# Kernel optimization log

Measured on AMD Instinct MI355X. Metric: run time of the kernel, lower is better.

The kernel has to match this reference:

```python
import jax, jax.numpy as jnp
import numpy as np
from jax import lax

B, N, HID, H, FFN, L, MHD = 16, 128, 768, 32, 3072, 12, 5
S = N + 1


def _ln(x, g, b):
    m = x.mean(-1, keepdims=True)
    v = ((x - m) ** 2).mean(-1, keepdims=True)
    return (x - m) * lax.rsqrt(v + 1e-5) * g + b


def setup_inputs() -> dict:
    key = jax.random.key(0)
    ks = jax.random.split(key, 32)
    f = lambda i, shape: jax.random.normal(ks[i], shape, jnp.float32) * 0.02
    z0 = lambda w: w.at[0].set(0.0)  # padding_idx=0 rows are zero
    inp = {}
    inp["attn_bias"] = jax.random.normal(ks[0], (B, S, S), jnp.float32)
    inp["spatial_pos"] = jax.random.randint(ks[1], (B, N, N), 0, 512)
    inp["x"] = jax.random.randint(ks[2], (B, N, 9), 0, 4608)
    inp["in_degree"] = jax.random.randint(ks[3], (B, N), 0, 512)
    inp["out_degree"] = jax.random.randint(ks[4], (B, N), 0, 512)
    inp["edge_input"] = jax.random.randint(ks[5], (B, N, N, MHD, 3), 0, 1536)
    inp["atom_emb"] = z0(f(6, (512 * 9 + 1, HID)))
    inp["edge_emb"] = z0(f(7, (512 * 3 + 1, H)))
    inp["edge_dis_emb"] = f(8, (128 * H * H, 1))
    inp["spatial_emb"] = z0(f(9, (512, H)))
    inp["in_deg_emb"] = z0(f(10, (512, HID)))
    inp["out_deg_emb"] = z0(f(11, (512, HID)))
    inp["graph_token"] = f(12, (1, HID))
    inp["gt_vd"] = f(13, (1, H))
    inp["ln1_g"] = jnp.ones((L, HID)); inp["ln1_b"] = jnp.zeros((L, HID))
    inp["wq"] = f(14, (L, HID, HID)); inp["bq"] = jnp.zeros((L, HID))
    inp["wk"] = f(15, (L, HID, HID)); inp["bk"] = jnp.zeros((L, HID))
    inp["wv"] = f(16, (L, HID, HID)); inp["bv"] = jnp.zeros((L, HID))
    inp["wo"] = f(17, (L, HID, HID)); inp["bo"] = jnp.zeros((L, HID))
    inp["ln2_g"] = jnp.ones((L, HID)); inp["ln2_b"] = jnp.zeros((L, HID))
    inp["w1"] = f(18, (L, HID, FFN)); inp["b1"] = jnp.zeros((L, FFN))
    inp["w2"] = f(19, (L, FFN, HID)); inp["b2"] = jnp.zeros((L, HID))
    inp["final_g"] = jnp.ones((HID,)); inp["final_b"] = jnp.zeros((HID,))
    inp["proj_w"] = f(20, (HID, 1)); inp["proj_b"] = jnp.zeros((1,))
    return inp


def _forward(attn_bias, spatial_pos, x, in_degree, out_degree, edge_input,
             atom_emb, edge_emb, edge_dis_emb, spatial_emb, in_deg_emb, out_deg_emb,
             graph_token, gt_vd, ln1_g, ln1_b, wq, bq, wk, bk, wv, bv, wo, bo,
             ln2_g, ln2_b, w1, b1, w2, b2, final_g, final_b, proj_w, proj_b):
    Bn = attn_bias.shape[0]
    # ---- graph attention bias [B,H,S,S] ----
    gab = jnp.broadcast_to(attn_bias[:, None], (Bn, H, S, S))
    sp_bias = spatial_emb[spatial_pos].transpose(0, 3, 1, 2)  # [B,H,N,N]
    gab = gab.at[:, :, 1:, 1:].add(sp_bias)
    t = gt_vd.reshape(1, H, 1)
    gab = gab.at[:, :, 1:, 0].add(t)
    gab = gab.at[:, :, 0, :].add(t)
    # ---- multi-hop edge bias ----
    sp = jnp.where(spatial_pos == 0, 1, spatial_pos)
    sp = jnp.where(sp > 1, sp - 1, sp)
    sp = jnp.clip(sp, 0, MHD)
    ei = edge_input[:, :, :, :MHD, :]                  # [B,N,N,D,3]
    ee = edge_emb[ei].mean(-2)                         # [B,N,N,D,H]
    D = ee.shape[3]
    flat = ee.transpose(3, 0, 1, 2, 4).reshape(D, -1, H)
    W = edge_dis_emb.reshape(-1, H, H)[:D]
    flat = jnp.einsum('dbh,dhk->dbk', flat, W)
    ee = flat.reshape(D, Bn, N, N, H).transpose(1, 2, 3, 0, 4)
    ee = ee.sum(-2) / sp.astype(ee.dtype)[..., None]   # [B,N,N,H]
    gab = gab.at[:, :, 1:, 1:].add(ee.transpose(0, 3, 1, 2))
    gab = gab + attn_bias[:, None]
    # ---- node features ----
    nf = atom_emb[x].sum(-2) + in_deg_emb[in_degree] + out_deg_emb[out_degree]
    gt = jnp.broadcast_to(graph_token[None], (Bn, 1, HID))
    h = jnp.concatenate([gt, nf], axis=1)              # [B,S,HID]
    d = HID // H
    scale = d ** -0.5

    def step(h, p):
        g1, b1_, Wq, Bq, Wk, Bk, Wv, Bv, Wo, Bo, g2, b2_, W1, B1, W2, B2 = p
        y = _ln(h, g1, b1_)
        q = (y @ Wq + Bq).reshape(Bn, S, H, d) * scale
        k = (y @ Wk + Bk).reshape(Bn, S, H, d)
        v = (y @ Wv + Bv).reshape(Bn, S, H, d)
        s = jnp.einsum('bqhd,bkhd->bhqk', q, k) + gab
        a = jax.nn.softmax(s, axis=-1)
        o = jnp.einsum('bhqk,bkhd->bqhd', a, v).reshape(Bn, S, HID) @ Wo + Bo
        h = h + o
        z = _ln(h, g2, b2_)
        z = jax.nn.gelu(z @ W1 + B1, approximate=False) @ W2 + B2
        return h + z, None

    h = lax.scan(step, h, (ln1_g, ln1_b, wq, bq, wk, bk, wv, bv, wo, bo,
                           ln2_g, ln2_b, w1, b1, w2, b2))[0]
    h = _ln(h, final_g, final_b)
    return h[:, 0, :] @ proj_w + proj_b                # [B, output_dim]


def reference(attn_bias, spatial_pos, x, in_degree, out_degree, edge_input,
              atom_emb, edge_emb, edge_dis_emb, spatial_emb, in_deg_emb, out_deg_emb,
              graph_token, gt_vd, ln1_g, ln1_b, wq, bq, wk, bk, wv, bv, wo, bo,
              ln2_g, ln2_b, w1, b1, w2, b2, final_g, final_b, proj_w, proj_b):
    return _forward(attn_bias, spatial_pos, x, in_degree, out_degree, edge_input,
                    atom_emb, edge_emb, edge_dis_emb, spatial_emb, in_deg_emb, out_deg_emb,
                    graph_token, gt_vd, ln1_g, ln1_b, wq, bq, wk, bk, wv, bv, wo, bo,
                    ln2_g, ln2_b, w1, b1, w2, b2, final_g, final_b, proj_w, proj_b)
```

## Files before the change

### kernel.cpp

```cpp
#include <hip/hip_runtime.h>
#include <hip/hip_bf16.h>
#include <math.h>

#define B_ 16
#define N_ 128
#define S_ 129
#define HID_ 768
#define H_ 32
#define D_ 24
#define FFN_ 3072
#define L_ 12
#define M_ (B_*S_)
#define SP_ 144
#define KP_ 160

#define WQKV_E ((size_t)2304*768)
#define WO_E   ((size_t)768*768)
#define W1_E   ((size_t)3072*768)
#define W2_E   ((size_t)768*3072)
#define WL_E_  (WQKV_E + WO_E + W1_E + W2_E)

typedef __attribute__((ext_vector_type(8))) short short8;
typedef __attribute__((ext_vector_type(4))) float f32x4;
typedef __hip_bfloat16 bf16;

#define VMCNT(n) asm volatile("s_waitcnt vmcnt(" #n ")" ::: "memory")
#define LDS_FENCE() asm volatile("" ::: "memory")

__device__ __forceinline__ void gload_lds16(const void* g, void* l) {
  __builtin_amdgcn_global_load_lds(
      (const __attribute__((address_space(1))) void*)g,
      (__attribute__((address_space(3))) void*)l, 16, 0, 0);
}

__device__ __forceinline__ float gld(const float* p) { return *p; }
__device__ __forceinline__ float gld(const bf16* p)  { return __bfloat162float(*p); }

__global__ __launch_bounds__(256) void gab_bound_kernel(
    const float* __restrict__ ab, const float* __restrict__ gtvd,
    float* __restrict__ gab, bf16* __restrict__ gabh)
{
  int u = blockIdx.x * 256 + threadIdx.x;
  const int PB = 2*S_ - 1;
  if (u >= B_*H_*PB) return;
  int p = u % PB;
  int bh = u / PB;
  int hh = bh % H_, b = bh / H_;
  int qi, kj;
  if (p < S_) { qi = 0; kj = p; } else { qi = p - S_ + 1; kj = 0; }
  float v = 2.0f * ab[(b*S_ + qi)*S_ + kj] + gtvd[hh];
  long g = ((long)(b*H_ + hh)*S_ + qi)*S_ + kj;
  if (gabh) gabh[g] = __float2bfloat16(v);
  else      gab[g]  = v;
}

__global__ __launch_bounds__(256) void ftab_kernel(
    const float* __restrict__ eemb, const float* __restrict__ edis,
    float* __restrict__ F)
{
  __shared__ float em[8][32];
  int tid = threadIdx.x;
  int jl = tid >> 5, hh = tid & 31;
  int p = blockIdx.x * 8 + jl;
  bool valid = p < 5*1537;
  int d = valid ? p / 1537 : 0;
  int idx = valid ? p % 1537 : 0;
  em[jl][hh] = eemb[idx*32 + hh];
  float acc = 0.f;
#pragma unroll
  for (int hp = 0; hp < 32; ++hp)
    acc += em[jl][hp] * edis[d*1024 + hp*32 + hh];
  if (valid) F[(long)p*32 + hh] = acc * (1.0f/3.0f);
}

__global__ __launch_bounds__(256) void edge_kernel(
    const int* __restrict__ eidx, const float* __restrict__ F,
    const int* __restrict__ spos, const float* __restrict__ spemb,
    const float* __restrict__ ab, float* __restrict__ gab,
    bf16* __restrict__ gabh)
{
  __shared__ float outj[128][33];
  int tid = threadIdx.x;
  int jl = tid >> 5, hh = tid & 31;
  int bi = blockIdx.x;
  int b = bi >> 7, i = bi & 127;
  const int* erow = eidx + ((long)((b*N_ + i)*N_)) * 15;

  int er[15];
#pragma unroll
  for (int t = 0; t < 15; ++t) er[t] = erow[jl*15 + t];

  for (int ch = 0; ch < 16; ++ch) {
    int j = ch*8 + jl;
    int ern[15];
    if (ch < 15) {
#pragma unroll
      for (int t = 0; t < 15; ++t) ern[t] = erow[(j+8)*15 + t];
    }
    float acc = 0.f;
#pragma unroll
    for (int t = 0; t < 15; ++t)
      acc += F[((long)((t/3)*1537 + er[t]))*32 + hh];
    int sp0 = spos[(b*N_ + i)*N_ + j];
    int sp = (sp0 == 0) ? 1 : sp0;
    if (sp > 1) sp -= 1;
    if (sp > 5) sp = 5;
    outj[j][hh] = spemb[sp0*H_ + hh] + acc / (float)sp;
    if (ch < 15) {
#pragma unroll
      for (int t = 0; t < 15; ++t) er[t] = ern[t];
    }
  }
  __syncthreads();
  {
    int c = tid & 127;
    float base = 2.0f * ab[((long)(b*S_) + (i+1))*S_ + 1 + c];
    for (int it = 0; it < 16; ++it) {
      int r = it*2 + (tid >> 7);
      float v = base + outj[c][r];
      long g = ((long)(b*H_ + r)*S_ + (i+1))*S_ + 1 + c;
      if (gabh) gabh[g] = __float2bfloat16(v);
      else      gab[g]  = v;
    }
  }
}

__global__ __launch_bounds__(256) void nodefeat_ln_kernel(
    const int* __restrict__ x, const int* __restrict__ indeg,
    const int* __restrict__ outdeg, const float* __restrict__ atom_emb,
    const float* __restrict__ in_emb, const float* __restrict__ out_emb,
    const float* __restrict__ gtok, const float* __restrict__ g,
    const float* __restrict__ bta, float* __restrict__ h,
    bf16* __restrict__ y)
{
  int row = blockIdx.x;
  int tid = threadIdx.x;
  int sidx = row % S_;
  int b = row / S_;
  float v[3];
  if (sidx == 0) {
#pragma unroll
    for (int j = 0; j < 3; ++j) v[j] = gtok[tid + j*256];
  } else {
    int n = sidx - 1;
    int id = indeg[b*N_ + n], od = outdeg[b*N_ + n];
    const int* xr = x + (b*N_ + n)*9;
    int xi[9];
#pragma unroll
    for (int e = 0; e < 9; ++e) xi[e] = xr[e];
#pragma unroll
    for (int j = 0; j < 3; ++j) {
      int c = tid + j*256;
      float a = in_emb[(long)id*HID_ + c] + out_emb[(long)od*HID_ + c];
#pragma unroll
      for (int e = 0; e < 9; ++e) a += atom_emb[(long)xi[e]*HID_ + c];
      v[j] = a;
    }
  }
  float* hr = h + (long)row*HID_;
#pragma unroll
  for (int j = 0; j < 3; ++j) hr[tid + j*256] = v[j];

  float s = v[0] + v[1] + v[2];
  float ss = v[0]*v[0] + v[1]*v[1] + v[2]*v[2];
  for (int off = 32; off > 0; off >>= 1) {
    s  += __shfl_xor(s, off);
    ss += __shfl_xor(ss, off);
  }
  __shared__ float rs[4], rss[4];
  int w = tid / 64;
  if ((tid & 63) == 0) { rs[w] = s; rss[w] = ss; }
  __syncthreads();
  s  = rs[0] + rs[1] + rs[2] + rs[3];
  ss = rss[0] + rss[1] + rss[2] + rss[3];
  float mean = s * (1.0f/768.0f);
  float var  = ss * (1.0f/768.0f) - mean*mean;
  float rstd = rsqrtf(var + 1e-5f);
  bf16* yr = y + (long)row*HID_;
#pragma unroll
  for (int j = 0; j < 3; ++j) {
    int c = tid + j*256;
    yr[c] = __float2bfloat16((v[j] - mean)*rstd*g[c] + bta[c]);
  }
}

__global__ __launch_bounds__(256) void ln_kernel(
    const float* __restrict__ in, const float* __restrict__ g,
    const float* __restrict__ bta, bf16* __restrict__ out)
{
  int row = blockIdx.x;
  int tid = threadIdx.x;
  const float* xr = in + (long)row * HID_;
  float x0 = xr[tid], x1 = xr[tid + 256], x2 = xr[tid + 512];
  float s = x0 + x1 + x2;
  float ss = x0*x0 + x1*x1 + x2*x2;
  for (int off = 32; off > 0; off >>= 1) {
    s  += __shfl_xor(s, off);
    ss += __shfl_xor(ss, off);
  }
  __shared__ float rs[4], rss[4];
  int w = tid / 64;
  if ((tid & 63) == 0) { rs[w] = s; rss[w] = ss; }
  __syncthreads();
  s  = rs[0] + rs[1] + rs[2] + rs[3];
  ss = rss[0] + rss[1] + rss[2] + rss[3];
  float mean = s * (1.0f/768.0f);
  float var  = ss * (1.0f/768.0f) - mean*mean;
  float rstd = rsqrtf(var + 1e-5f);
  bf16* orow = out + (long)row * HID_;
  orow[tid]       = __float2bfloat16((x0 - mean)*rstd*g[tid]       + bta[tid]);
  orow[tid + 256] = __float2bfloat16((x1 - mean)*rstd*g[tid + 256] + bta[tid + 256]);
  orow[tid + 512] = __float2bfloat16((x2 - mean)*rstd*g[tid + 512] + bta[tid + 512]);
}

template<int NZ>
__global__ __launch_bounds__(256) void addln_kernel(
    const float* __restrict__ part, const float* __restrict__ bias,
    const float* __restrict__ g, const float* __restrict__ bta,
    float* __restrict__ h, bf16* __restrict__ y)
{
  int row = blockIdx.x;
  int tid = threadIdx.x;
  const long MN = (long)M_*HID_;
  float* hr = h + (long)row*HID_;
  float v[3];
#pragma unroll
  for (int j = 0; j < 3; ++j) {
    int c = tid + j*256;
    float a = hr[c] + bias[c];
    const float* pp = part + (long)row*HID_ + c;
#pragma unroll
    for (int z = 0; z < NZ; ++z) a += pp[(long)z*MN];
    v[j] = a;
    hr[c] = a;
  }
  float s = v[0] + v[1] + v[2];
  float ss = v[0]*v[0] + v[1]*v[1] + v[2]*v[2];
  for (int off = 32; off > 0; off >>= 1) {
    s  += __shfl_xor(s, off);
    ss += __shfl_xor(ss, off);
  }
  __shared__ float rs[4], rss[4];
  int w = tid / 64;
  if ((tid & 63) == 0) { rs[w] = s; rss[w] = ss; }
  __syncthreads();
  s  = rs[0] + rs[1] + rs[2] + rs[3];
  ss = rss[0] + rss[1] + rss[2] + rss[3];
  float mean = s * (1.0f/768.0f);
  float var  = ss * (1.0f/768.0f) - mean*mean;
  float rstd = rsqrtf(var + 1e-5f);
  bf16* yr = y + (long)row*HID_;
#pragma unroll
  for (int j = 0; j < 3; ++j) {
    int c = tid + j*256;
    yr[c] = __float2bfloat16((v[j] - mean)*rstd*g[c] + bta[c]);
  }
}

__global__ __launch_bounds__(256) void wconv_kernel(
    const float* __restrict__ W, bf16* __restrict__ Out,
    int K, int N, float scale)
{
  __shared__ float tile[32][33];
  int bx = blockIdx.x * 32;
  int by = blockIdx.y * 32;
  int tx = threadIdx.x & 31, ty = threadIdx.x >> 5;
#pragma unroll
  for (int r = 0; r < 32; r += 8)
    tile[ty + r][tx] = W[(long)(by + ty + r)*N + bx + tx];
  __syncthreads();
#pragma unroll
  for (int r = 0; r < 32; r += 8)
    Out[(long)(bx + ty + r)*K + by + tx] = __float2bfloat16(tile[tx][ty + r] * scale);
}

__global__ __launch_bounds__(256) void qkvconv_kernel(
    const float* __restrict__ wq, const float* __restrict__ wk,
    const float* __restrict__ wv, bf16* __restrict__ Out, float scale)
{
  const float* W = blockIdx.z == 0 ? wq : blockIdx.z == 1 ? wk : wv;
  float sc = blockIdx.z == 0 ? scale : 1.0f;
  __shared__ float tile[32][33];
  int bx = blockIdx.x * 32;
  int by = blockIdx.y * 32;
  int tx = threadIdx.x & 31, ty = threadIdx.x >> 5;
#pragma unroll
  for (int r = 0; r < 32; r += 8)
    tile[ty + r][tx] = W[(long)(by + ty + r)*768 + bx + tx];
  __syncthreads();
  bf16* O = Out + (long)blockIdx.z * 768 * 768;
#pragma unroll
  for (int r = 0; r < 32; r += 8)
    O[(long)(bx + ty + r)*768 + by + tx] = __float2bfloat16(tile[tx][ty + r] * sc);
}

__global__ __launch_bounds__(256) void qkvconv_all_kernel(
    const float* __restrict__ wq, const float* __restrict__ wk,
    const float* __restrict__ wv, bf16* __restrict__ wbuf, float scale)
{
  int z = blockIdx.z;
  int l = z / 3, which = z % 3;
  const float* W = (which == 0 ? wq : which == 1 ? wk : wv) + (size_t)l*768*768;
  float sc = which == 0 ? scale : 1.0f;
  __shared__ float tile[32][33];
  int bx = blockIdx.x * 32;
  int by = blockIdx.y * 32;
  int tx = threadIdx.x & 31, ty = threadIdx.x >> 5;
#pragma unroll
  for (int r = 0; r < 32; r += 8)
    tile[ty + r][tx] = W[(long)(by + ty + r)*768 + bx + tx];
  __syncthreads();
  bf16* O = wbuf + (size_t)l*WL_E_ + (size_t)which*768*768;
#pragma unroll
  for (int r = 0; r < 32; r += 8)
    O[(long)(bx + ty + r)*768 + by + tx] = __float2bfloat16(tile[tx][ty + r] * sc);
}

__global__ __launch_bounds__(256) void wconv_all_kernel(
    const float* __restrict__ Wb, bf16* __restrict__ Ob,
    int K, int N, long inStride, long outStride)
{
  int z = blockIdx.z;
  const float* W = Wb + (size_t)z * inStride;
  bf16* Out = Ob + (size_t)z * outStride;
  __shared__ float tile[32][33];
  int bx = blockIdx.x * 32;
  int by = blockIdx.y * 32;
  int tx = threadIdx.x & 31, ty = threadIdx.x >> 5;
#pragma unroll
  for (int r = 0; r < 32; r += 8)
    tile[ty + r][tx] = W[(long)(by + ty + r)*N + bx + tx];
  __syncthreads();
#pragma unroll
  for (int r = 0; r < 32; r += 8)
    Out[(long)(bx + ty + r)*K + by + tx] = __float2bfloat16(tile[tx][ty + r]);
}

__global__ __launch_bounds__(256) void biasqkv_kernel(
    const float* __restrict__ bq, const float* __restrict__ bk,
    const float* __restrict__ bv, float* __restrict__ bqkv, float scale)
{
  int idx = blockIdx.x * 256 + threadIdx.x;
  if (idx >= L_*2304) return;
  int l = idx / 2304, n = idx % 2304;
  int p = n / 768, nn = n % 768;
  float v = (p == 0) ? bq[l*768 + nn]*scale : (p == 1) ? bk[l*768 + nn] : bv[l*768 + nn];
  bqkv[idx] = v;
}

__device__ __forceinline__ void stage64k(
    const bf16* __restrict__ A, const bf16* __restrict__ Wt,
    bf16* Als, bf16* Bls, int bm, int bn, long ka, int M, int lda, int ldb, int tid)
{
  int r0 = tid >> 3, c = tid & 7;
#pragma unroll
  for (int p = 0; p < 2; ++p) {
    int row = p*32 + r0;
    int cs = c ^ (row & 7);
    int grow = bm + row; if (grow >= M) grow = M - 1;
    gload_lds16(A + (long)grow*lda + ka + cs*8, Als + (p*256 + (tid & ~63))*8);
    gload_lds16(Wt + (long)(bn + row)*ldb + ka + cs*8, Bls + (p*256 + (tid & ~63))*8);
  }
}

__global__ __launch_bounds__(256) void gemm64_kernel(
    const bf16* __restrict__ A, const bf16* __restrict__ Wt,
    const float* __restrict__ bias, const float* __restrict__ resid,
    void* __restrict__ Cout, int M, int N, int Klen, int lda, int ldb, int mode)
{
  constexpr int ASZ = 64*64;
  __shared__ bf16 Als[2*ASZ];
  __shared__ bf16 Bls[2*ASZ];
  int tid = threadIdx.x;
  int wid = tid >> 6, lane = tid & 63;

  int gx = gridDim.x;
  int nwg = gx * gridDim.y;
  int id = blockIdx.y * gx + blockIdx.x;
  int q = nwg >> 3, r = nwg & 7;
  int xcd = id & 7, off = id >> 3;
  int swz = (xcd < r) ? (xcd*(q+1) + off) : (r*(q+1) + (xcd - r)*q + off);
  int bm = (swz / gx) * 64, bn = (swz % gx) * 64;

  long koff = (long)blockIdx.z * Klen;
  int wr = wid >> 1, wc = wid & 1;
  int lr = lane & 15, kg = lane >> 4;

  int aoff[2][2], boff[2][2];
#pragma unroll
  for (int m = 0; m < 2; ++m) {
    int row = wr*32 + m*16 + lr;
#pragma unroll
    for (int hf = 0; hf < 2; ++hf) {
      int chunk = hf*4 + kg;
      aoff[m][hf] = (row*8 + (chunk ^ (row & 7)))*8;
    }
  }
#pragma unroll
  for (int n = 0; n < 2; ++n) {
    int col = wc*32 + n*16 + lr;
#pragma unroll
    for (int hf = 0; hf < 2; ++hf) {
      int chunk = hf*4 + kg;
      boff[n][hf] = (col*8 + (chunk ^ (col & 7)))*8;
    }
  }

  f32x4 acc[2][2];
#pragma unroll
  for (int m = 0; m < 2; ++m)
#pragma unroll
    for (int n = 0; n < 2; ++n)
      acc[m][n] = (f32x4){0.0f, 0.0f, 0.0f, 0.0f};

  int nt = Klen >> 6;
  stage64k(A, Wt, Als,       Bls,       bm, bn, koff,      M, lda, ldb, tid);
  stage64k(A, Wt, Als + ASZ, Bls + ASZ, bm, bn, koff + 64, M, lda, ldb, tid);

  int cur = 0;
  for (int t = 0; t < nt; ++t) {
    if (t + 1 < nt) VMCNT(4);
    else            VMCNT(0);
    __builtin_amdgcn_s_barrier();
    LDS_FENCE();
    bf16* Acur = Als + cur*ASZ;
    bf16* Bcur = Bls + cur*ASZ;
    short8 av[2][2], bv2[2][2];
#pragma unroll
    for (int m = 0; m < 2; ++m)
#pragma unroll
      for (int hf = 0; hf < 2; ++hf) av[m][hf] = *(const short8*)(Acur + aoff[m][hf]);
#pragma unroll
    for (int n = 0; n < 2; ++n)
#pragma unroll
      for (int hf = 0; hf < 2; ++hf) bv2[n][hf] = *(const short8*)(Bcur + boff[n][hf]);
#pragma unroll
    for (int hf = 0; hf < 2; ++hf)
#pragma unroll
      for (int m = 0; m < 2; ++m)
#pragma unroll
        for (int n = 0; n < 2; ++n)
          acc[m][n] = __builtin_amdgcn_mfma_f32_16x16x32_bf16(av[m][hf], bv2[n][hf], acc[m][n], 0, 0, 0);
    LDS_FENCE();
    __builtin_amdgcn_s_barrier();
    if (t + 2 < nt)
      stage64k(A, Wt, Als + cur*ASZ, Bls + cur*ASZ,
               bm, bn, koff + (long)(t+2)*64, M, lda, ldb, tid);
    cur ^= 1;
  }

#pragma unroll
  for (int n = 0; n < 2; ++n) {
    int col = bn + wc*32 + n*16 + lr;
    float bcol = (mode == 3) ? 0.0f : bias[col];
#pragma unroll
    for (int m = 0; m < 2; ++m) {
      f32x4 a = acc[m][n];
#pragma unroll
      for (int i = 0; i < 4; ++i) {
        int row = bm + wr*32 + m*16 + kg*4 + i;
        if (row < M) {
          float v = a[i] + bcol;
          if (mode == 1) v = 0.5f * v * (1.0f + erff(v * 0.70710678118654752f));
          if (mode == 2)
            ((float*)Cout)[(long)row*N + col] = v + resid[(long)row*N + col];
          else if (mode == 3)
            ((float*)Cout + (size_t)blockIdx.z*M*N)[(long)row*N + col] = v;
          else
            ((bf16*)Cout)[(long)row*N + col] = __float2bfloat16(v);
        }
      }
    }
  }
}

template<typename GT>
__global__ __launch_bounds__(512) void attn_kernel(
    const bf16* __restrict__ qkv, const GT* __restrict__ gab,
    bf16* __restrict__ ob)
{
  int bh = blockIdx.x;
  int b = bh >> 5, hh = bh & 31;
  __shared__ bf16 kl[SP_*32];
  __shared__ bf16 vt[32*KP_];
  __shared__ bf16 pl[8][16*KP_];
  int tid = threadIdx.x;
  int wv = tid >> 6, lane = tid & 63;
  const short8 z8 = (short8){0,0,0,0,0,0,0,0};

  for (int idx = tid; idx < 32*KP_/8; idx += 512)
    *(short8*)&vt[idx*8] = z8;
  const bf16* qbase = qkv + (long)b*S_*2304 + hh*24;
  for (int u = tid; u < SP_*4; u += 512) {
    int row = u >> 2, c8 = u & 3;
    short8 kv = z8;
    if (row < S_ && c8 < 3)
      kv = *(const short8*)(qbase + (long)row*2304 + 768 + c8*8);
    int cs = c8 ^ ((row >> 1) & 3);
    *(short8*)&kl[row*32 + cs*8] = kv;
  }
  __syncthreads();
  for (int u = tid; u < S_*3; u += 512) {
    int kj = u / 3, c8 = u % 3;
    short8 vv = *(const short8*)(qbase + (long)kj*2304 + 1536 + c8*8);
    int kb = kj & 7, kh = kj >> 3;
#pragma unroll
    for (int e = 0; e < 8; ++e) {
      int c = c8*8 + e;
      int ch = kh ^ ((c >> 1) & 3);
      short sv = vv[e];
      vt[c*KP_ + ch*8 + kb] = *reinterpret_cast<bf16*>(&sv);
    }
  }
  __syncthreads();

  int l15 = lane & 15, l4 = lane >> 4;

  short8 bvf[5][2];
#pragma unroll
  for (int kc = 0; kc < 5; ++kc)
#pragma unroll
    for (int ntc = 0; ntc < 2; ++ntc) {
      int col = ntc*16 + l15;
      int ch = (kc*4 + l4) ^ ((col >> 1) & 3);
      bvf[kc][ntc] = *(const short8*)&vt[col*KP_ + ch*8];
    }

  bf16* plw = pl[wv];
  for (int idx = lane; idx < 16*KP_/8; idx += 64)
    *(short8*)&plw[idx*8] = z8;

  const GT* gb = gab + (long)(b*H_ + hh)*S_*S_;

  for (int rep = 0; rep < 2; ++rep) {
    int mf = (rep == 0) ? wv : ((wv == 0) ? 8 : -1);
    if (mf < 0) continue;
    int qb0 = mf * 16;
    int qrow = qb0 + l15;
    short8 aq = z8;
    if (qrow < S_ && l4 < 3)
      aq = *(const short8*)(qbase + (long)qrow*2304 + l4*8);
    f32x4 sc[9];
#pragma unroll
    for (int nt = 0; nt < 9; ++nt) {
      int krow = nt*16 + l15;
      int kch = l4 ^ ((krow >> 1) & 3);
      short8 bk = *(const short8*)&kl[krow*32 + kch*8];
      sc[nt] = __builtin_amdgcn_mfma_f32_16x16x32_bf16(aq, bk, (f32x4){0,0,0,0}, 0, 0, 0);
    }
    float mx[4] = {-1e30f,-1e30f,-1e30f,-1e30f};
#pragma unroll
    for (int nt = 0; nt < 9; ++nt) {
      int kj = nt*16 + l15;
      int kjc = kj < S_ ? kj : 0;
#pragma unroll
      for (int i = 0; i < 4; ++i) {
        int q = qb0 + l4*4 + i;
        int qc = q < S_ ? q : 0;
        float v = sc[nt][i] + gld(&gb[(long)qc*S_ + kjc]);
        if (kj >= S_) v = -1e30f;
        sc[nt][i] = v;
        mx[i] = fmaxf(mx[i], v);
      }
    }
#pragma unroll
    for (int i = 0; i < 4; ++i) {
      mx[i] = fmaxf(mx[i], __shfl_xor(mx[i], 1));
      mx[i] = fmaxf(mx[i], __shfl_xor(mx[i], 2));
      mx[i] = fmaxf(mx[i], __shfl_xor(mx[i], 4));
      mx[i] = fmaxf(mx[i], __shfl_xor(mx[i], 8));
    }
    float sum[4] = {0.f,0.f,0.f,0.f};
#pragma unroll
    for (int nt = 0; nt < 9; ++nt)
#pragma unroll
      for (int i = 0; i < 4; ++i) {
        float e = __expf(sc[nt][i] - mx[i]);
        sc[nt][i] = e;
        sum[i] += e;
      }
#pragma unroll
    for (int i = 0; i < 4; ++i) {
      sum[i] += __shfl_xor(sum[i], 1);
      sum[i] += __shfl_xor(sum[i], 2);
      sum[i] += __shfl_xor(sum[i], 4);
      sum[i] += __shfl_xor(sum[i], 8);
    }
#pragma unroll
    for (int nt = 0; nt < 9; ++nt) {
      int kj = nt*16 + l15;
#pragma unroll
      for (int i = 0; i < 4; ++i) {
        int q = l4*4 + i;
        int ch = (kj >> 3) ^ ((q >> 1) & 3);
        plw[q*KP_ + ch*8 + (kj & 7)] = __float2bfloat16(sc[nt][i]);
      }
    }
    f32x4 av[2] = {(f32x4){0,0,0,0}, (f32x4){0,0,0,0}};
#pragma unroll
    for (int kc = 0; kc < 5; ++kc) {
      int ch = (kc*4 + l4) ^ ((l15 >> 1) & 3);
      short8 ap = *(const short8*)&plw[l15*KP_ + ch*8];
#pragma unroll
      for (int ntc = 0; ntc < 2; ++ntc)
        av[ntc] = __builtin_amdgcn_mfma_f32_16x16x32_bf16(ap, bvf[kc][ntc], av[ntc], 0, 0, 0);
    }
#pragma unroll
    for (int ntc = 0; ntc < 2; ++ntc) {
      int c = ntc*16 + l15;
      if (c < 24) {
#pragma unroll
        for (int i = 0; i < 4; ++i) {
          int q = qb0 + l4*4 + i;
          if (q < S_)
            ob[(long)(b*S_ + q)*768 + hh*24 + c] = __float2bfloat16(av[ntc][i] / sum[i]);
        }
      }
    }
  }
}

__global__ __launch_bounds__(256) void final_kernel(
    const float* __restrict__ h, const float* __restrict__ fg,
    const float* __restrict__ fb, const float* __restrict__ pw,
    const float* __restrict__ pb, float* __restrict__ out)
{
  int b = blockIdx.x;
  int tid = threadIdx.x;
  const float* xr = h + (long)b * S_ * HID_;
  float x0 = xr[tid], x1 = xr[tid + 256], x2 = xr[tid + 512];
  float s = x0 + x1 + x2;
  float ss = x0*x0 + x1*x1 + x2*x2;
  for (int off = 32; off > 0; off >>= 1) {
    s  += __shfl_xor(s, off);
    ss += __shfl_xor(ss, off);
  }
  __shared__ float rs[4], rss[4], rd[4];
  int w = tid / 64;
  if ((tid & 63) == 0) { rs[w] = s; rss[w] = ss; }
  __syncthreads();
  s  = rs[0] + rs[1] + rs[2] + rs[3];
  ss = rss[0] + rss[1] + rss[2] + rss[3];
  float mean = s * (1.0f/768.0f);
  float var  = ss * (1.0f/768.0f) - mean*mean;
  float rstd = rsqrtf(var + 1e-5f);
  float d0 = ((x0 - mean)*rstd*fg[tid]       + fb[tid])       * pw[tid];
  float d1 = ((x1 - mean)*rstd*fg[tid + 256] + fb[tid + 256]) * pw[tid + 256];
  float d2 = ((x2 - mean)*rstd*fg[tid + 512] + fb[tid + 512]) * pw[tid + 512];
  float pd = d0 + d1 + d2;
  for (int off = 32; off > 0; off >>= 1) pd += __shfl_xor(pd, off);
  if ((tid & 63) == 0) rd[w] = pd;
  __syncthreads();
  if (tid == 0) out[b] = rd[0] + rd[1] + rd[2] + rd[3] + pb[0];
}

extern "C" void kernel_launch(void* const* d_in, const int* in_sizes, int n_in,
                              void* d_out, int out_size, void* d_ws, size_t ws_size,
                              hipStream_t stream)
{
  const float* attn_bias   = (const float*)d_in[0];
  const int*   spatial_pos = (const int*)d_in[1];
  const int*   x           = (const int*)d_in[2];
  const int*   in_degree   = (const int*)d_in[3];
  const int*   out_degree  = (const int*)d_in[4];
  const int*   edge_input  = (const int*)d_in[5];
  const float* atom_emb    = (const float*)d_in[6];
  const float* edge_emb    = (const float*)d_in[7];
  const float* edge_dis    = (const float*)d_in[8];
  const float* spatial_emb = (const float*)d_in[9];
  const float* in_deg_emb  = (const float*)d_in[10];
  const float* out_deg_emb = (const float*)d_in[11];
  const float* graph_token = (const float*)d_in[12];
  const float* gt_vd       = (const float*)d_in[13];
  const float* ln1_g = (const float*)d_in[14];
  const float* ln1_b = (const float*)d_in[15];
  const float* wq = (const float*)d_in[16];
  const float* bq = (const float*)d_in[17];
  const float* wk = (const float*)d_in[18];
  const float* bk = (const float*)d_in[19];
  const float* wv = (const float*)d_in[20];
  const float* bv = (const float*)d_in[21];
  const float* wo = (const float*)d_in[22];
  const float* bo = (const float*)d_in[23];
  const float* ln2_g = (const float*)d_in[24];
  const float* ln2_b = (const float*)d_in[25];
  const float* w1 = (const float*)d_in[26];
  const float* b1 = (const float*)d_in[27];
  const float* w2 = (const float*)d_in[28];
  const float* b2 = (const float*)d_in[29];
  const float* final_g = (const float*)d_in[30];
  const float* final_b = (const float*)d_in[31];
  const float* proj_w  = (const float*)d_in[32];
  const float* proj_b  = (const float*)d_in[33];

  float* out = (float*)d_out;

  const float scale = 0.20412414523193154f;
  const long GAB_N = (long)B_*H_*S_*S_;
  const size_t PART_B = (size_t)4 * M_ * 768 * 4;

  char* dws = (char*)d_ws;
  char* p = dws;
  float* gab  = (float*)p;  p += GAB_N*4;
  float* h    = (float*)p;  p += (long)M_*HID_*4;
  bf16*  y    = (bf16*)p;   p += (long)M_*HID_*2;
  bf16*  qkv  = (bf16*)p;
  bf16*  ffn  = qkv;
  p += (long)M_*2304*2;
  bf16*  ob   = (bf16*)p;   p += (long)M_*HID_*2;
  float* Ftab = (float*)p;  p += (long)5*1537*32*4;
  float* bqkv = (float*)p;  p += (long)L_*2304*4;

  float* part = (float*)p;
  bool psplit = ws_size >= (size_t)(p - dws) + PART_B + WL_E_*2;
  if (psplit) p += PART_B;
  bf16* gabh = (bf16*)p;
  bool g16 = ws_size >= (size_t)(p - dws) + (size_t)GAB_N*2 + WL_E_*2;
  if (g16) p += GAB_N*2;
  bf16* wbuf = (bf16*)p;
  bool full = ws_size >= (size_t)(p - dws) + (size_t)L_ * WL_E_ * 2;

  const int PB = 2*S_ - 1;
  gab_bound_kernel<<<(B_*H_*PB + 255)/256, 256, 0, stream>>>(
      attn_bias, gt_vd, gab, g16 ? gabh : nullptr);
  ftab_kernel<<<(5*1537 + 7)/8, 256, 0, stream>>>(edge_emb, edge_dis, Ftab);
  edge_kernel<<<B_*N_, 256, 0, stream>>>(
      edge_input, Ftab, spatial_pos, spatial_emb, attn_bias, gab,
      g16 ? gabh : nullptr);
  nodefeat_ln_kernel<<<M_, 256, 0, stream>>>(
      x, in_degree, out_degree, atom_emb, in_deg_emb, out_deg_emb, graph_token,
      ln1_g, ln1_b, h, y);
  biasqkv_kernel<<<(L_*2304 + 255)/256, 256, 0, stream>>>(bq, bk, bv, bqkv, scale);

  if (full) {
    qkvconv_all_kernel<<<dim3(24,24,3*L_), 256, 0, stream>>>(wq, wk, wv, wbuf, scale);
    wconv_all_kernel<<<dim3(24,24,L_), 256, 0, stream>>>(
        wo, wbuf + WQKV_E, 768, 768, (long)768*768, (long)WL_E_);
    wconv_all_kernel<<<dim3(96,24,L_), 256, 0, stream>>>(
        w1, wbuf + WQKV_E + WO_E, 768, 3072, (long)768*3072, (long)WL_E_);
    wconv_all_kernel<<<dim3(24,96,L_), 256, 0, stream>>>(
        w2, wbuf + WQKV_E + WO_E + W1_E, 3072, 768, (long)3072*768, (long)WL_E_);
  }

  const int MT = (M_ + 63)/64;
  dim3 gQKV(2304/64, MT);
  dim3 gO  (768/64,  MT);
  dim3 gO2 (768/64,  MT, 2);
  dim3 gF1 (3072/64, MT);
  dim3 gF2 (768/64,  MT, 4);
  dim3 cQKV(768/32, 768/32, 3);
  dim3 cO  (768/32, 768/32);
  dim3 cW1 (3072/32, 768/32);
  dim3 cW2 (768/32, 3072/32);

  auto wptr = [&](int l) { return wbuf + (full ? (size_t)l : 0) * WL_E_; };
  auto conv = [&](int l) {
    bf16* W = wptr(l);
    qkvconv_kernel<<<cQKV, 256, 0, stream>>>(
        wq + (size_t)l*HID_*HID_, wk + (size_t)l*HID_*HID_, wv + (size_t)l*HID_*HID_,
        W, scale);
    wconv_kernel<<<cO, 256, 0, stream>>>(wo + (size_t)l*HID_*HID_, W + WQKV_E, 768, 768, 1.0f);
    wconv_kernel<<<cW1, 256, 0, stream>>>(w1 + (size_t)l*HID_*FFN_, W + WQKV_E + WO_E, 768, 3072, 1.0f);
    wconv_kernel<<<cW2, 256, 0, stream>>>(w2 + (size_t)l*FFN_*HID_, W + WQKV_E + WO_E + W1_E, 3072, 768, 1.0f);
  };

  for (int l = 0; l < L_; ++l) {
    if (!full) conv(l);
    bf16* W = wptr(l);
    bf16* Wqkvt = W;
    bf16* Wot   = W + WQKV_E;
    bf16* W1t   = W + WQKV_E + WO_E;
    bf16* W2t   = W + WQKV_E + WO_E + W1_E;

    if (l > 0 && !psplit)
      ln_kernel<<<M_, 256, 0, stream>>>(h, ln1_g + l*HID_, ln1_b + l*HID_, y);

    gemm64_kernel<<<gQKV, 256, 0, stream>>>(
        y, Wqkvt, bqkv + l*2304, nullptr, qkv, M_, 2304, 768, 768, 768, 0);
    if (g16)
      attn_kernel<bf16><<<B_*H_, 512, 0, stream>>>(qkv, gabh, ob);
    else
      attn_kernel<float><<<B_*H_, 512, 0, stream>>>(qkv, gab, ob);

    if (psplit) {
      gemm64_kernel<<<gO2, 256, 0, stream>>>(
          ob, Wot, nullptr, nullptr, part, M_, 768, 384, 768, 768, 3);
      addln_kernel<2><<<M_, 256, 0, stream>>>(
          part, bo + l*HID_, ln2_g + l*HID_, ln2_b + l*HID_, h, y);
    } else {
      gemm64_kernel<<<gO, 256, 0, stream>>>(
          ob, Wot, bo + l*HID_, h, h, M_, 768, 768, 768, 768, 2);
      ln_kernel<<<M_, 256, 0, stream>>>(h, ln2_g + l*HID_, ln2_b + l*HID_, y);
    }

    gemm64_kernel<<<gF1, 256, 0, stream>>>(
        y, W1t, b1 + l*FFN_, nullptr, ffn, M_, 3072, 768, 768, 768, 1);

    if (psplit) {
      gemm64_kernel<<<gF2, 256, 0, stream>>>(
          ffn, W2t, nullptr, nullptr, part, M_, 768, 768, 3072, 3072, 3);
      int ln = (l + 1 < L_) ? l + 1 : 0;
      addln_kernel<4><<<M_, 256, 0, stream>>>(
          part, b2 + l*HID_, ln1_g + ln*HID_, ln1_b + ln*HID_, h, y);
    } else {
      gemm64_kernel<<<gO, 256, 0, stream>>>(
          ffn, W2t, b2 + l*HID_, h, h, M_, 768, 3072, 3072, 3072, 2);
    }
  }

  final_kernel<<<B_, 256, 0, stream>>>(h, final_g, final_b, proj_w, proj_b, out);
}
```

Before: 1.640 ms.

## Add 128x128-tile GEMM kernel for QKV and FFN1 projections

Introduces a 512-thread GEMM kernel with 128x128 output tiles, double-buffered LDS staging via direct global-to-LDS loads, XOR-swizzled LDS layout, and an XCD-aware block remap. It replaces the 64x64 GEMM for the wide QKV and first FFN projections to raise operand reuse per tile and reduce global/LDS traffic per MFMA. The cost is fewer workgroups (17 row tiles times 18 or 24 column tiles), which may under-fill the GPU, plus higher register and LDS use per block.

```diff
diff --git a/kernel.cpp b/kernel.cpp
--- a/kernel.cpp
+++ b/kernel.cpp
@@ -468,6 +468,126 @@
             ((float*)Cout + (size_t)blockIdx.z*M*N)[(long)row*N + col] = v;
           else
             ((bf16*)Cout)[(long)row*N + col] = __float2bfloat16(v);
+        }
+      }
+    }
+  }
+}
+
+__device__ __forceinline__ void stage128k(
+    const bf16* __restrict__ A, const bf16* __restrict__ Wt,
+    bf16* Als, bf16* Bls, int bm, int bn, long ka, int M, int lda, int ldb, int tid)
+{
+  int r0 = tid >> 3, c = tid & 7;
+#pragma unroll
+  for (int p = 0; p < 2; ++p) {
+    int row = p*64 + r0;
+    int cs = c ^ (row & 7);
+    int grow = bm + row; if (grow >= M) grow = M - 1;
+    gload_lds16(A + (long)grow*lda + ka + cs*8, Als + (p*512 + (tid & ~63))*8);
+    gload_lds16(Wt + (long)(bn + row)*ldb + ka + cs*8, Bls + (p*512 + (tid & ~63))*8);
+  }
+}
+
+__global__ __launch_bounds__(512) void gemm128_kernel(
+    const bf16* __restrict__ A, const bf16* __restrict__ Wt,
+    const float* __restrict__ bias, void* __restrict__ Cout,
+    int M, int N, int Klen, int lda, int ldb, int mode)
+{
+  constexpr int ASZ = 128*64;
+  __shared__ bf16 Als[2*ASZ];
+  __shared__ bf16 Bls[2*ASZ];
+  int tid = threadIdx.x;
+  int wid = tid >> 6, lane = tid & 63;
+
+  int gx = gridDim.x;
+  int nwg = gx * gridDim.y;
+  int id = blockIdx.y * gx + blockIdx.x;
+  int q = nwg >> 3, r = nwg & 7;
+  int xcd = id & 7, off = id >> 3;
+  int swz = (xcd < r) ? (xcd*(q+1) + off) : (r*(q+1) + (xcd - r)*q + off);
+  int bm = (swz / gx) * 128, bn = (swz % gx) * 128;
+
+  int wr = wid >> 2, wc = wid & 3;
+  int lr = lane & 15, kg = lane >> 4;
+
+  int aoff[4][2], boff[2][2];
+#pragma unroll
+  for (int m = 0; m < 4; ++m) {
+    int row = wr*64 + m*16 + lr;
+#pragma unroll
+    for (int hf = 0; hf < 2; ++hf) {
+      int chunk = hf*4 + kg;
+      aoff[m][hf] = (row*8 + (chunk ^ (row & 7)))*8;
+    }
+  }
+#pragma unroll
+  for (int n = 0; n < 2; ++n) {
+    int col = wc*32 + n*16 + lr;
+#pragma unroll
+    for (int hf = 0; hf < 2; ++hf) {
+      int chunk = hf*4 + kg;
+      boff[n][hf] = (col*8 + (chunk ^ (col & 7)))*8;
+    }
+  }
+
+  f32x4 acc[4][2];
+#pragma unroll
+  for (int m = 0; m < 4; ++m)
+#pragma unroll
+    for (int n = 0; n < 2; ++n)
+      acc[m][n] = (f32x4){0.0f, 0.0f, 0.0f, 0.0f};
+
+  int nt = Klen >> 6;
+  stage128k(A, Wt, Als,       Bls,       bm, bn, 0,  M, lda, ldb, tid);
+  stage128k(A, Wt, Als + ASZ, Bls + ASZ, bm, bn, 64, M, lda, ldb, tid);
+
+  int cur = 0;
+  for (int t = 0; t < nt; ++t) {
+    if (t + 1 < nt) VMCNT(4);
+    else            VMCNT(0);
+    __builtin_amdgcn_s_barrier();
+    LDS_FENCE();
+    bf16* Acur = Als + cur*ASZ;
+    bf16* Bcur = Bls + cur*ASZ;
+    short8 av[4][2], bv2[2][2];
+#pragma unroll
+    for (int m = 0; m < 4; ++m)
+#pragma unroll
+      for (int hf = 0; hf < 2; ++hf) av[m][hf] = *(const short8*)(Acur + aoff[m][hf]);
+#pragma unroll
+    for (int n = 0; n < 2; ++n)
+#pragma unroll
+      for (int hf = 0; hf < 2; ++hf) bv2[n][hf] = *(const short8*)(Bcur + boff[n][hf]);
+#pragma unroll
+    for (int hf = 0; hf < 2; ++hf)
+#pragma unroll
+      for (int m = 0; m < 4; ++m)
+#pragma unroll
+        for (int n = 0; n < 2; ++n)
+          acc[m][n] = __builtin_amdgcn_mfma_f32_16x16x32_bf16(av[m][hf], bv2[n][hf], acc[m][n], 0, 0, 0);
+    LDS_FENCE();
+    __builtin_amdgcn_s_barrier();
+    if (t + 2 < nt)
+      stage128k(A, Wt, Als + cur*ASZ, Bls + cur*ASZ,
+                bm, bn, (long)(t+2)*64, M, lda, ldb, tid);
+    cur ^= 1;
+  }
+
+#pragma unroll
+  for (int n = 0; n < 2; ++n) {
+    int col = bn + wc*32 + n*16 + lr;
+    float bcol = bias[col];
+#pragma unroll
+    for (int m = 0; m < 4; ++m) {
+      f32x4 a = acc[m][n];
+#pragma unroll
+      for (int i = 0; i < 4; ++i) {
+        int row = bm + wr*64 + m*16 + kg*4 + i;
+        if (row < M) {
+          float v = a[i] + bcol;
+          if (mode == 1) v = 0.5f * v * (1.0f + erff(v * 0.70710678118654752f));
+          ((bf16*)Cout)[(long)row*N + col] = __float2bfloat16(v);
         }
       }
     }
@@ -742,11 +862,12 @@
         w2, wbuf + WQKV_E + WO_E + W1_E, 3072, 768, (long)3072*768, (long)WL_E_);
   }
 
-  const int MT = (M_ + 63)/64;
-  dim3 gQKV(2304/64, MT);
+  const int MT  = (M_ + 63)/64;
+  const int MT2 = (M_ + 127)/128;
+  dim3 gQKV(2304/128, MT2);
+  dim3 gF1 (3072/128, MT2);
+  dim3 gO2 (768/64,  MT, 2);
   dim3 gO  (768/64,  MT);
-  dim3 gO2 (768/64,  MT, 2);
-  dim3 gF1 (3072/64, MT);
   dim3 gF2 (768/64,  MT, 4);
   dim3 cQKV(768/32, 768/32, 3);
   dim3 cO  (768/32, 768/32);
@@ -775,8 +896,8 @@
     if (l > 0 && !psplit)
       ln_kernel<<<M_, 256, 0, stream>>>(h, ln1_g + l*HID_, ln1_b + l*HID_, y);
 
-    gemm64_kernel<<<gQKV, 256, 0, stream>>>(
-        y, Wqkvt, bqkv + l*2304, nullptr, qkv, M_, 2304, 768, 768, 768, 0);
+    gemm128_kernel<<<gQKV, 512, 0, stream>>>(
+        y, Wqkvt, bqkv + l*2304, qkv, M_, 2304, 768, 768, 768, 0);
     if (g16)
       attn_kernel<bf16><<<B_*H_, 512, 0, stream>>>(qkv, gabh, ob);
     else
@@ -793,8 +914,8 @@
       ln_kernel<<<M_, 256, 0, stream>>>(h, ln2_g + l*HID_, ln2_b + l*HID_, y);
     }
 
-    gemm64_kernel<<<gF1, 256, 0, stream>>>(
-        y, W1t, b1 + l*FFN_, nullptr, ffn, M_, 3072, 768, 768, 768, 1);
+    gemm128_kernel<<<gF1, 512, 0, stream>>>(
+        y, W1t, b1 + l*FFN_, ffn, M_, 3072, 768, 768, 768, 1);
 
     if (psplit) {
       gemm64_kernel<<<gF2, 256, 0, stream>>>(
```

Measured after the change: 1.571 ms. -4.2%, faster.
